# Kernel tuning notes

Measured on AMD Instinct MI355X. Metric: run time of the kernel, lower is better.

The kernel has to match this reference:

```python
import jax, jax.numpy as jnp
import numpy as np

D_MODEL = 1024
N_HEADS = 16


def setup_inputs() -> dict:
    key = jax.random.key(0)
    ks = jax.random.split(key, 5)
    B, T, C = 4, 2048, D_MODEL
    x = jax.random.normal(ks[0], (B, T, C), dtype=jnp.float32)
    W_attn = jax.random.normal(ks[1], (C, 3 * C), dtype=jnp.float32) * (1.0 / np.sqrt(C))
    b_attn = jnp.zeros((3 * C,), dtype=jnp.float32)
    W_proj = jax.random.normal(ks[2], (C, C), dtype=jnp.float32) * (1.0 / np.sqrt(C))
    b_proj = jnp.zeros((C,), dtype=jnp.float32)
    return {"x": x, "W_attn": W_attn, "b_attn": b_attn, "W_proj": W_proj, "b_proj": b_proj}


def reference(x, W_attn, b_attn, W_proj, b_proj):
    B, T, C = x.shape
    H = N_HEADS
    hd = C // H
    qkv = x @ W_attn + b_attn                      # [B,T,3C]
    q, k, v = jnp.split(qkv, 3, axis=2)
    # [B,T,C] -> [B,H,T,hd]
    q = q.reshape(B, T, H, hd).transpose(0, 2, 1, 3)
    k = k.reshape(B, T, H, hd).transpose(0, 2, 1, 3)
    v = v.reshape(B, T, H, hd).transpose(0, 2, 1, 3)
    scale = 1.0 / jnp.sqrt(jnp.float32(hd))
    attn = jnp.einsum('bhqd,bhkd->bhqk', q, k) * scale
    causal = jnp.tril(jnp.ones((T, T), dtype=bool))
    attn = jnp.where(causal[None, None], attn, -jnp.inf)
    w = jax.nn.softmax(attn, axis=-1)
    ctx = jnp.einsum('bhqk,bhkd->bhqd', w, v)      # [B,H,T,hd]
    ctx = ctx.transpose(0, 2, 1, 3).reshape(B, T, C)
    return ctx @ W_proj + b_proj
```

## Files before the change

kernel.cpp:

```cpp
#include <hip/hip_runtime.h>
#include <hip/hip_bf16.h>

typedef __bf16 bf16x8 __attribute__((ext_vector_type(8)));
typedef __bf16 bf16x4 __attribute__((ext_vector_type(4)));
typedef float f32x4 __attribute__((ext_vector_type(4)));

#define MFMA(A, B, C) __builtin_amdgcn_mfma_f32_16x16x32_bf16((A), (B), (C), 0, 0, 0)

#if __has_builtin(__builtin_amdgcn_exp2f)
#define EXP2(x) __builtin_amdgcn_exp2f(x)
#else
#define EXP2(x) exp2f(x)
#endif

#define T_SEQ 2048
#define BATCH 4
#define CDIM  1024
#define HEADS 16
#define HD    64
#define MROWS (BATCH * T_SEQ)
#define QK_SCALE 0.18033688011112042f
#define KTILES (CDIM / 64)

__device__ __forceinline__ void async_ld16(const __bf16* g, __bf16* l) {
    __builtin_amdgcn_global_load_lds(
        (const __attribute__((address_space(1))) void*)g,
        (__attribute__((address_space(3))) void*)l, 16, 0, 0);
}

__global__ __launch_bounds__(256) void prep(const float* __restrict__ x,
                                            __bf16* __restrict__ xbf,
                                            const float* __restrict__ Wa,
                                            __bf16* __restrict__ Wat,
                                            const float* __restrict__ Wp,
                                            __bf16* __restrict__ qkv)
{
    __shared__ float tile[32][33];
    const int bid = blockIdx.x;
    if (bid < 4096) {
        long i = ((long)bid * 256 + threadIdx.x) * 8;
        f32x4 f0 = ((const f32x4*)(x + i))[0];
        f32x4 f1 = ((const f32x4*)(x + i))[1];
        bf16x8 v;
#pragma unroll
        for (int j = 0; j < 4; j++) { v[j] = (__bf16)f0[j]; v[4 + j] = (__bf16)f1[j]; }
        *(bf16x8*)(xbf + i) = v;
    } else if (bid < 7168) {
        const int bb = bid - 4096;
        const int tx = threadIdx.x & 31, ty = threadIdx.x >> 5;
        const int c0 = (bb % 96) * 32, r0 = (bb / 96) * 32;
#pragma unroll
        for (int i = 0; i < 4; i++)
            tile[ty + i * 8][tx] = Wa[(long)(r0 + ty + i * 8) * (3 * CDIM) + c0 + tx];
        __syncthreads();
#pragma unroll
        for (int i = 0; i < 4; i++)
            Wat[(long)(c0 + ty + i * 8) * CDIM + r0 + tx] = (__bf16)tile[tx][ty + i * 8];
    } else {
        const int bb = bid - 7168;
        const int tx = threadIdx.x & 31, ty = threadIdx.x >> 5;
        const int c0 = (bb % 32) * 32, r0 = (bb / 32) * 32;
#pragma unroll
        for (int i = 0; i < 4; i++)
            tile[ty + i * 8][tx] = Wp[(long)(r0 + ty + i * 8) * CDIM + c0 + tx];
        __syncthreads();
#pragma unroll
        for (int i = 0; i < 4; i++)
            qkv[(long)(c0 + ty + i * 8) * (3 * CDIM) + 2 * CDIM + r0 + tx] =
                (__bf16)tile[tx][ty + i * 8];
    }
}


#define QS_ALO(p, kt)                                                            \
    do {                                                                         \
        async_ld16(Asrc + (long)(kt) * 64, &Ab[p][sdst]);                        \
        async_ld16(Asrc + (long)128 * CDIM + (kt) * 64, &Ab[p][8192 + sdst]);    \
    } while (0)
#define QS_AHI(p, kt)                                                            \
    do {                                                                         \
        async_ld16(Asrc + (long)64 * CDIM + (kt) * 64, &Ab[p][4096 + sdst]);     \
        async_ld16(Asrc + (long)192 * CDIM + (kt) * 64, &Ab[p][12288 + sdst]);   \
    } while (0)
#define QS_B(p, kt)                                                              \
    do {                                                                         \
        async_ld16(Bsrc + (long)(kt) * 64, &Bb[p][sdst]);                        \
        async_ld16(Bsrc + (long)64 * CDIM + (kt) * 64, &Bb[p][4096 + sdst]);     \
        async_ld16(Bsrc + (long)128 * CDIM + (kt) * 64, &Bb[p][8192 + sdst]);    \
    } while (0)

__global__ __launch_bounds__(512, 2) void gemm_qkv(const __bf16* __restrict__ A,
                                                   const __bf16* __restrict__ Bt,
                                                   const float* __restrict__ bias,
                                                   __bf16* __restrict__ C,
                                                   __bf16* __restrict__ vt)
{
    __shared__ __attribute__((aligned(16))) __bf16 Ab[2][256 * 64];
    __shared__ __attribute__((aligned(16))) __bf16 Bb[2][192 * 64];

    const int bid = (int)blockIdx.x;
    const int swz = (bid & 7) * 64 + (bid >> 3);
    const int n0 = (swz & 15) * 192;
    const int m0 = (swz >> 4) * 256;

    const int t = threadIdx.x;
    const int wave = t >> 6, lane = t & 63;
    const int quad = lane >> 4, l15 = lane & 15;
    const int wm = wave >> 2, wn = wave & 3;

    const int srow = t >> 3;
    const int scol = ((t & 7) * 8) ^ ((srow & 7) << 3);
    const int sdst = srow * 64 + (t & 7) * 8;
    const __bf16* Asrc = A + (long)(m0 + srow) * CDIM + scol;
    const __bf16* Bsrc = Bt + (long)(n0 + srow) * CDIM + scol;

    const int kx0 = (quad * 8) ^ ((l15 & 7) << 3);
    const int kx1 = (32 + quad * 8) ^ ((l15 & 7) << 3);
    const int aro = (wm * 128 + l15) * 64;
    const int bro = (wn * 48 + l15) * 64;

    f32x4 acc[8][3] = {};
    bf16x8 A0[4][2], A1[4][2], B0[2][2], B1[2];

    QS_ALO(0, 0); QS_AHI(0, 0); QS_B(0, 0);
    QS_ALO(1, 1); QS_AHI(1, 1); QS_B(1, 1);
    asm volatile("s_waitcnt vmcnt(7)" ::: "memory");
    __builtin_amdgcn_s_barrier();
#pragma unroll
    for (int mf = 0; mf < 4; mf++) {
        A0[mf][0] = *(const bf16x8*)&Ab[0][aro + mf * 1024 + kx0];
        A0[mf][1] = *(const bf16x8*)&Ab[0][aro + mf * 1024 + kx1];
    }
#pragma unroll
    for (int nf = 0; nf < 2; nf++) {
        B0[nf][0] = *(const bf16x8*)&Bb[0][bro + nf * 1024 + kx0];
        B0[nf][1] = *(const bf16x8*)&Bb[0][bro + nf * 1024 + kx1];
    }

#pragma unroll 2
    for (int kt = 0; kt < KTILES; ++kt) {
        const int cur = kt & 1, nxt = cur ^ 1;

#pragma unroll
        for (int mf = 0; mf < 4; mf++) {
            A1[mf][0] = *(const bf16x8*)&Ab[cur][aro + 4096 + mf * 1024 + kx0];
            A1[mf][1] = *(const bf16x8*)&Ab[cur][aro + 4096 + mf * 1024 + kx1];
        }
        B1[0] = *(const bf16x8*)&Bb[cur][bro + 2048 + kx0];
        B1[1] = *(const bf16x8*)&Bb[cur][bro + 2048 + kx1];
        asm volatile("s_waitcnt lgkmcnt(10)" ::: "memory");
        __builtin_amdgcn_sched_barrier(0);
        __builtin_amdgcn_s_setprio(1);
#pragma unroll
        for (int mf = 0; mf < 4; mf++)
#pragma unroll
            for (int nf = 0; nf < 2; nf++) {
                acc[mf][nf] = MFMA(A0[mf][0], B0[nf][0], acc[mf][nf]);
                acc[mf][nf] = MFMA(A0[mf][1], B0[nf][1], acc[mf][nf]);
            }
        __builtin_amdgcn_s_setprio(0);
        asm volatile("s_waitcnt lgkmcnt(0)" ::: "memory");
        __builtin_amdgcn_sched_barrier(0);
        __builtin_amdgcn_s_setprio(1);
#pragma unroll
        for (int mf = 0; mf < 4; mf++)
#pragma unroll
            for (int nf = 0; nf < 2; nf++) {
                acc[4 + mf][nf] = MFMA(A1[mf][0], B0[nf][0], acc[4 + mf][nf]);
                acc[4 + mf][nf] = MFMA(A1[mf][1], B0[nf][1], acc[4 + mf][nf]);
            }
        __builtin_amdgcn_s_setprio(0);
        asm volatile("s_waitcnt vmcnt(0)" ::: "memory");
        __builtin_amdgcn_s_barrier();

        __builtin_amdgcn_s_setprio(1);
#pragma unroll
        for (int mf = 0; mf < 4; mf++) {
            acc[mf][2] = MFMA(A0[mf][0], B1[0], acc[mf][2]);
            acc[mf][2] = MFMA(A0[mf][1], B1[1], acc[mf][2]);
        }
        __builtin_amdgcn_s_setprio(0);
        if (kt + 1 < KTILES) {
#pragma unroll
            for (int mf = 0; mf < 4; mf++) {
                A0[mf][0] = *(const bf16x8*)&Ab[nxt][aro + mf * 1024 + kx0];
                A0[mf][1] = *(const bf16x8*)&Ab[nxt][aro + mf * 1024 + kx1];
            }
#pragma unroll
            for (int nf = 0; nf < 2; nf++) {
                B0[nf][0] = *(const bf16x8*)&Bb[nxt][bro + nf * 1024 + kx0];
                B0[nf][1] = *(const bf16x8*)&Bb[nxt][bro + nf * 1024 + kx1];
            }
        }
        if (kt + 2 < KTILES) { QS_ALO(cur, kt + 2); QS_AHI(cur, kt + 2); QS_B(cur, kt + 2); }
        __builtin_amdgcn_s_setprio(1);
#pragma unroll
        for (int mf = 0; mf < 4; mf++) {
            acc[4 + mf][2] = MFMA(A1[mf][0], B1[0], acc[4 + mf][2]);
            acc[4 + mf][2] = MFMA(A1[mf][1], B1[1], acc[4 + mf][2]);
        }
        __builtin_amdgcn_s_setprio(0);
    }

    const int bB = m0 >> 11;
    const int tb = (m0 & (T_SEQ - 1)) + wm * 128;
#pragma unroll
    for (int mf = 0; mf < 8; mf++) {
#pragma unroll
        for (int nf = 0; nf < 3; nf++) {
            const int colb = n0 + wn * 48 + nf * 16;
            const int col = colb + l15;
            const float bv = bias[col];
            if (colb >= 2 * CDIM) {
                __bf16* vdst = vt + (long)(bB * CDIM + col - 2 * CDIM) * T_SEQ
                             + tb + (mf >> 2) * 64 + (mf & 3) * 16 + quad * 4;
                bf16x4 pv;
#pragma unroll
                for (int r = 0; r < 4; r++) pv[r] = (__bf16)(acc[mf][nf][r] + bv);
                *(bf16x4*)vdst = pv;
            } else {
                const float sc = (col < CDIM) ? QK_SCALE : 1.0f;
#pragma unroll
                for (int r = 0; r < 4; r++) {
                    const int row = m0 + wm * 128 + (mf >> 2) * 64 + (mf & 3) * 16 + quad * 4 + r;
                    C[(long)row * (3 * CDIM) + col] = (__bf16)((acc[mf][nf][r] + bv) * sc);
                }
            }
        }
    }
}

#define PS_A(p, kt)                                                              \
    do {                                                                         \
        async_ld16(Asrc + (long)(kt) * 64, &Ab[p][sdst]);                        \
        async_ld16(Asrc + (long)64 * (3 * CDIM) + (kt) * 64, &Ab[p][4096 + sdst]); \
    } while (0)
#define PS_B(p, kt)                                                              \
    do {                                                                         \
        async_ld16(Bsrc + (long)(kt) * 64, &Bb[p][sdst]);                        \
        async_ld16(Bsrc + (long)64 * (3 * CDIM) + (kt) * 64, &Bb[p][4096 + sdst]); \
        async_ld16(Bsrc + (long)128 * (3 * CDIM) + (kt) * 64, &Bb[p][8192 + sdst]); \
        async_ld16(Bsrc + (long)192 * (3 * CDIM) + (kt) * 64, &Bb[p][12288 + sdst]); \
    } while (0)

__global__ __launch_bounds__(512, 2) void gemm_proj(const __bf16* __restrict__ A,
                                                    const float* __restrict__ bias,
                                                    float* __restrict__ C)
{
    __shared__ __attribute__((aligned(16))) __bf16 Ab[2][128 * 64];
    __shared__ __attribute__((aligned(16))) __bf16 Bb[2][256 * 64];

    const int bid = (int)blockIdx.x;
    const int swz = (bid & 7) * 32 + (bid >> 3);
    const int n0 = (swz & 3) * 256;
    const int m0 = (swz >> 2) * 128;

    const int t = threadIdx.x;
    const int wave = t >> 6, lane = t & 63;
    const int quad = lane >> 4, l15 = lane & 15;
    const int wm = wave >> 2, wn = wave & 3;

    const int srow = t >> 3;
    const int scol = ((t & 7) * 8) ^ ((srow & 7) << 3);
    const int sdst = srow * 64 + (t & 7) * 8;
    const __bf16* Asrc = A + (long)(m0 + srow) * (3 * CDIM) + scol;
    const __bf16* Bsrc = A + (long)(n0 + srow) * (3 * CDIM) + 2 * CDIM + scol;

    const int kx0 = (quad * 8) ^ ((l15 & 7) << 3);
    const int kx1 = (32 + quad * 8) ^ ((l15 & 7) << 3);
    const int aro = (wm * 64 + l15) * 64;
    const int bro = (wn * 64 + l15) * 64;

    f32x4 acc[4][4] = {};
    bf16x8 A0[2][2], A1[2][2], B0[2][2], B1[2][2];

    PS_A(0, 0); PS_B(0, 0);
    PS_A(1, 1); PS_B(1, 1);
    asm volatile("s_waitcnt vmcnt(6)" ::: "memory");
    __builtin_amdgcn_s_barrier();
#pragma unroll
    for (int mf = 0; mf < 2; mf++) {
        A0[mf][0] = *(const bf16x8*)&Ab[0][aro + mf * 1024 + kx0];
        A0[mf][1] = *(const bf16x8*)&Ab[0][aro + mf * 1024 + kx1];
    }
#pragma unroll
    for (int nf = 0; nf < 2; nf++) {
        B0[nf][0] = *(const bf16x8*)&Bb[0][bro + nf * 1024 + kx0];
        B0[nf][1] = *(const bf16x8*)&Bb[0][bro + nf * 1024 + kx1];
    }

#pragma unroll 2
    for (int kt = 0; kt < KTILES; ++kt) {
        const int cur = kt & 1, nxt = cur ^ 1;

#pragma unroll
        for (int mf = 0; mf < 2; mf++) {
            A1[mf][0] = *(const bf16x8*)&Ab[cur][aro + 2048 + mf * 1024 + kx0];
            A1[mf][1] = *(const bf16x8*)&Ab[cur][aro + 2048 + mf * 1024 + kx1];
        }
#pragma unroll
        for (int nf = 0; nf < 2; nf++) {
            B1[nf][0] = *(const bf16x8*)&Bb[cur][bro + 2048 + nf * 1024 + kx0];
            B1[nf][1] = *(const bf16x8*)&Bb[cur][bro + 2048 + nf * 1024 + kx1];
        }
        asm volatile("s_waitcnt lgkmcnt(8)" ::: "memory");
        __builtin_amdgcn_sched_barrier(0);
        __builtin_amdgcn_s_setprio(1);
#pragma unroll
        for (int mf = 0; mf < 2; mf++)
#pragma unroll
            for (int nf = 0; nf < 2; nf++) {
                acc[mf][nf] = MFMA(A0[mf][0], B0[nf][0], acc[mf][nf]);
                acc[mf][nf] = MFMA(A0[mf][1], B0[nf][1], acc[mf][nf]);
            }
        __builtin_amdgcn_s_setprio(0);
        asm volatile("s_waitcnt lgkmcnt(0)" ::: "memory");
        __builtin_amdgcn_sched_barrier(0);
        __builtin_amdgcn_s_setprio(1);
#pragma unroll
        for (int mf = 0; mf < 2; mf++)
#pragma unroll
            for (int nf = 0; nf < 2; nf++) {
                acc[2 + mf][nf] = MFMA(A1[mf][0], B0[nf][0], acc[2 + mf][nf]);
                acc[2 + mf][nf] = MFMA(A1[mf][1], B0[nf][1], acc[2 + mf][nf]);
            }
        __builtin_amdgcn_s_setprio(0);
        asm volatile("s_waitcnt vmcnt(0)" ::: "memory");
        __builtin_amdgcn_s_barrier();

        __builtin_amdgcn_s_setprio(1);
#pragma unroll
        for (int mf = 0; mf < 2; mf++)
#pragma unroll
            for (int nf = 0; nf < 2; nf++) {
                acc[mf][2 + nf] = MFMA(A0[mf][0], B1[nf][0], acc[mf][2 + nf]);
                acc[mf][2 + nf] = MFMA(A0[mf][1], B1[nf][1], acc[mf][2 + nf]);
            }
        __builtin_amdgcn_s_setprio(0);
        if (kt + 1 < KTILES) {
#pragma unroll
            for (int mf = 0; mf < 2; mf++) {
                A0[mf][0] = *(const bf16x8*)&Ab[nxt][aro + mf * 1024 + kx0];
                A0[mf][1] = *(const bf16x8*)&Ab[nxt][aro + mf * 1024 + kx1];
            }
#pragma unroll
            for (int nf = 0; nf < 2; nf++) {
                B0[nf][0] = *(const bf16x8*)&Bb[nxt][bro + nf * 1024 + kx0];
                B0[nf][1] = *(const bf16x8*)&Bb[nxt][bro + nf * 1024 + kx1];
            }
        }
        if (kt + 2 < KTILES) { PS_A(cur, kt + 2); PS_B(cur, kt + 2); }
        __builtin_amdgcn_s_setprio(1);
#pragma unroll
        for (int mf = 0; mf < 2; mf++)
#pragma unroll
            for (int nf = 0; nf < 2; nf++) {
                acc[2 + mf][2 + nf] = MFMA(A1[mf][0], B1[nf][0], acc[2 + mf][2 + nf]);
                acc[2 + mf][2 + nf] = MFMA(A1[mf][1], B1[nf][1], acc[2 + mf][2 + nf]);
            }
        __builtin_amdgcn_s_setprio(0);
    }

#pragma unroll
    for (int mf = 0; mf < 4; mf++) {
#pragma unroll
        for (int nf = 0; nf < 4; nf++) {
            const int col = n0 + wn * 64 + (nf >> 1) * 32 + (nf & 1) * 16 + l15;
            const float bv = bias[col];
#pragma unroll
            for (int r = 0; r < 4; r++) {
                const int row = m0 + wm * 64 + (mf >> 1) * 32 + (mf & 1) * 16 + quad * 4 + r;
                C[(long)row * CDIM + col] = acc[mf][nf][r] + bv;
            }
        }
    }
}

__global__ __launch_bounds__(256) void attn_kernel(__bf16* qkv,
                                                   const __bf16* __restrict__ vt)
{
    __shared__ __attribute__((aligned(16))) __bf16 Ks[2][64 * 32];
    __shared__ __attribute__((aligned(16))) __bf16 Vts[2][64 * 32];
    __shared__ __attribute__((aligned(16))) __bf16 Ps[8][16 * 72];

    const int bh = blockIdx.x;
    const int b = bh >> 4, h = bh & 15;
    const int qt = (int)gridDim.y - 1 - (int)blockIdx.y;
    const int q0 = qt * 128;
    const int t = threadIdx.x;
    const int wave = t >> 6, lane = t & 63;
    const int quad = lane >> 4, l15 = lane & 15;

    bf16x8 qfr[2][2];
#pragma unroll
    for (int f = 0; f < 2; f++) {
        const __bf16* qb = qkv + (long)(b * T_SEQ + q0 + f * 64 + wave * 16 + l15) * (3 * CDIM) + h * HD;
        qfr[f][0] = *(const bf16x8*)(qb + quad * 8);
        qfr[f][1] = *(const bf16x8*)(qb + 32 + quad * 8);
    }

    bf16x8 vone;
#pragma unroll
    for (int j = 0; j < 8; j++) vone[j] = (__bf16)1.0f;

    f32x4 Oacc[2][4] = {};
    f32x4 lacc[2] = {};

    const __bf16* kbase = qkv + (long)(b * T_SEQ + (t >> 2)) * (3 * CDIM)
                          + CDIM + h * HD + (t & 3) * 8;
    const __bf16* vbase = vt + ((long)bh * HD + (t >> 2)) * T_SEQ + (t & 3) * 8;

    const int ntiles = (q0 + 128) / 64;
    for (int kt = 0; kt < ntiles; kt++) {
        const __bf16* kp = kbase + (long)kt * 64 * (3 * CDIM);
        async_ld16(kp,      &Ks[0][t * 8]);
        async_ld16(kp + 32, &Ks[1][t * 8]);
        const __bf16* vp = vbase + kt * 64;
        async_ld16(vp,      &Vts[0][t * 8]);
        async_ld16(vp + 32, &Vts[1][t * 8]);
        __syncthreads();

#pragma unroll
        for (int c = 0; c < 4; c++) {
            bf16x8 kf0 = *(const bf16x8*)&Ks[0][(c * 16 + l15) * 32 + quad * 8];
            bf16x8 kf1 = *(const bf16x8*)&Ks[1][(c * 16 + l15) * 32 + quad * 8];
#pragma unroll
            for (int f = 0; f < 2; f++) {
                f32x4 z = {};
                z = MFMA(kf0, qfr[f][0], z);
                z = MFMA(kf1, qfr[f][1], z);
                const int qbf = q0 + f * 64 + wave * 16;
                const int qg = qbf + l15;
                const int kvb = kt * 64 + c * 16 + quad * 4;
                bf16x4 pk;
                if (kt * 64 + 63 > qbf) {
#pragma unroll
                    for (int r = 0; r < 4; r++) {
                        float v = (kvb + r > qg) ? -1e30f : z[r];
                        pk[r] = (__bf16)EXP2(v);
                    }
                } else {
#pragma unroll
                    for (int r = 0; r < 4; r++)
                        pk[r] = (__bf16)EXP2(z[r]);
                }
                *(bf16x4*)&Ps[wave * 2 + f][l15 * 72 + c * 16 + quad * 4] = pk;
            }
        }

        __threadfence_block();

        bf16x8 pf[2][2];
#pragma unroll
        for (int f = 0; f < 2; f++) {
            pf[f][0] = *(const bf16x8*)&Ps[wave * 2 + f][l15 * 72 + quad * 8];
            pf[f][1] = *(const bf16x8*)&Ps[wave * 2 + f][l15 * 72 + 32 + quad * 8];
            lacc[f] = MFMA(pf[f][0], vone, lacc[f]);
            lacc[f] = MFMA(pf[f][1], vone, lacc[f]);
        }
#pragma unroll
        for (int n = 0; n < 4; n++) {
            bf16x8 vf0 = *(const bf16x8*)&Vts[0][(n * 16 + l15) * 32 + quad * 8];
            bf16x8 vf1 = *(const bf16x8*)&Vts[1][(n * 16 + l15) * 32 + quad * 8];
#pragma unroll
            for (int f = 0; f < 2; f++) {
                Oacc[f][n] = MFMA(pf[f][0], vf0, Oacc[f][n]);
                Oacc[f][n] = MFMA(pf[f][1], vf1, Oacc[f][n]);
            }
        }
        __syncthreads();
    }

#pragma unroll
    for (int f = 0; f < 2; f++)
#pragma unroll
        for (int n = 0; n < 4; n++) {
            int col = h * HD + n * 16 + l15;
#pragma unroll
            for (int r = 0; r < 4; r++) {
                int row = q0 + f * 64 + wave * 16 + quad * 4 + r;
                float val = Oacc[f][n][r] / lacc[f][r];
                qkv[(long)(b * T_SEQ + row) * (3 * CDIM) + col] = (__bf16)val;
            }
        }
}

extern "C" void kernel_launch(void* const* d_in, const int* in_sizes, int n_in,
                              void* d_out, int out_size, void* d_ws, size_t ws_size,
                              hipStream_t stream) {
    (void)in_sizes; (void)n_in; (void)out_size; (void)ws_size;
    const float* x  = (const float*)d_in[0];
    const float* Wa = (const float*)d_in[1];
    const float* ba = (const float*)d_in[2];
    const float* Wp = (const float*)d_in[3];
    const float* bp = (const float*)d_in[4];
    float* out = (float*)d_out;

    char* ws = (char*)d_ws;
    __bf16* qkv = (__bf16*)(ws);
    __bf16* vt  = (__bf16*)(ws + 50331648);
    __bf16* xbf = (__bf16*)d_out;
    __bf16* Wat = (__bf16*)((char*)d_out + 16777216);

    prep<<<dim3(8192), 256, 0, stream>>>(x, xbf, Wa, Wat, Wp, qkv);

    gemm_qkv<<<dim3(512), 512, 0, stream>>>(xbf, Wat, ba, qkv, vt);

    attn_kernel<<<dim3(BATCH * HEADS, T_SEQ / 128), 256, 0, stream>>>(qkv, vt);

    gemm_proj<<<dim3(256), 512, 0, stream>>>(qkv, bp, out);
}
```

Measured before the change: 230.6 us.

## Double-buffer K/V tiles in attention kernel with async prefetch two ahead

```diff
diff --git a/kernel.cpp b/kernel.cpp
--- a/kernel.cpp
+++ b/kernel.cpp
@@ -376,11 +376,21 @@
     }
 }
 
-__global__ __launch_bounds__(256) void attn_kernel(__bf16* qkv,
-                                                   const __bf16* __restrict__ vt)
+#define ATT_STAGE(p, kt_)                                                        \
+    do {                                                                         \
+        const __bf16* kp_ = kbase + (long)(kt_) * 64 * (3 * CDIM);               \
+        async_ld16(kp_,      &Ks[p][0][t * 8]);                                  \
+        async_ld16(kp_ + 32, &Ks[p][1][t * 8]);                                  \
+        const __bf16* vp_ = vbase + (kt_) * 64;                                  \
+        async_ld16(vp_,      &Vts[p][0][t * 8]);                                 \
+        async_ld16(vp_ + 32, &Vts[p][1][t * 8]);                                 \
+    } while (0)
+
+__global__ __launch_bounds__(256, 3) void attn_kernel(__bf16* qkv,
+                                                      const __bf16* __restrict__ vt)
 {
-    __shared__ __attribute__((aligned(16))) __bf16 Ks[2][64 * 32];
-    __shared__ __attribute__((aligned(16))) __bf16 Vts[2][64 * 32];
+    __shared__ __attribute__((aligned(16))) __bf16 Ks[2][2][64 * 32];
+    __shared__ __attribute__((aligned(16))) __bf16 Vts[2][2][64 * 32];
     __shared__ __attribute__((aligned(16))) __bf16 Ps[8][16 * 72];
 
     const int bh = blockIdx.x;
@@ -411,19 +421,19 @@
     const __bf16* vbase = vt + ((long)bh * HD + (t >> 2)) * T_SEQ + (t & 3) * 8;
 
     const int ntiles = (q0 + 128) / 64;
+
+    ATT_STAGE(0, 0);
+    ATT_STAGE(1, 1);
+    asm volatile("s_waitcnt vmcnt(4)" ::: "memory");
+    __builtin_amdgcn_s_barrier();
+
     for (int kt = 0; kt < ntiles; kt++) {
-        const __bf16* kp = kbase + (long)kt * 64 * (3 * CDIM);
-        async_ld16(kp,      &Ks[0][t * 8]);
-        async_ld16(kp + 32, &Ks[1][t * 8]);
-        const __bf16* vp = vbase + kt * 64;
-        async_ld16(vp,      &Vts[0][t * 8]);
-        async_ld16(vp + 32, &Vts[1][t * 8]);
-        __syncthreads();
+        const int cur = kt & 1;
 
 #pragma unroll
         for (int c = 0; c < 4; c++) {
-            bf16x8 kf0 = *(const bf16x8*)&Ks[0][(c * 16 + l15) * 32 + quad * 8];
-            bf16x8 kf1 = *(const bf16x8*)&Ks[1][(c * 16 + l15) * 32 + quad * 8];
+            bf16x8 kf0 = *(const bf16x8*)&Ks[cur][0][(c * 16 + l15) * 32 + quad * 8];
+            bf16x8 kf1 = *(const bf16x8*)&Ks[cur][1][(c * 16 + l15) * 32 + quad * 8];
 #pragma unroll
             for (int f = 0; f < 2; f++) {
                 f32x4 z = {};
@@ -455,20 +465,33 @@
         for (int f = 0; f < 2; f++) {
             pf[f][0] = *(const bf16x8*)&Ps[wave * 2 + f][l15 * 72 + quad * 8];
             pf[f][1] = *(const bf16x8*)&Ps[wave * 2 + f][l15 * 72 + 32 + quad * 8];
+        }
+        bf16x8 vf[4][2];
+#pragma unroll
+        for (int n = 0; n < 4; n++) {
+            vf[n][0] = *(const bf16x8*)&Vts[cur][0][(n * 16 + l15) * 32 + quad * 8];
+            vf[n][1] = *(const bf16x8*)&Vts[cur][1][(n * 16 + l15) * 32 + quad * 8];
+        }
+        asm volatile("s_waitcnt lgkmcnt(0)" ::: "memory");
+        __builtin_amdgcn_sched_barrier(0);
+        asm volatile("s_waitcnt vmcnt(0)" ::: "memory");
+        __builtin_amdgcn_s_barrier();
+
+        if (kt + 2 < ntiles) ATT_STAGE(cur, kt + 2);
+        __builtin_amdgcn_s_setprio(1);
+#pragma unroll
+        for (int f = 0; f < 2; f++) {
             lacc[f] = MFMA(pf[f][0], vone, lacc[f]);
             lacc[f] = MFMA(pf[f][1], vone, lacc[f]);
         }
 #pragma unroll
-        for (int n = 0; n < 4; n++) {
-            bf16x8 vf0 = *(const bf16x8*)&Vts[0][(n * 16 + l15) * 32 + quad * 8];
-            bf16x8 vf1 = *(const bf16x8*)&Vts[1][(n * 16 + l15) * 32 + quad * 8];
+        for (int n = 0; n < 4; n++)
 #pragma unroll
             for (int f = 0; f < 2; f++) {
-                Oacc[f][n] = MFMA(pf[f][0], vf0, Oacc[f][n]);
-                Oacc[f][n] = MFMA(pf[f][1], vf1, Oacc[f][n]);
-            }
-        }
-        __syncthreads();
+                Oacc[f][n] = MFMA(pf[f][0], vf[n][0], Oacc[f][n]);
+                Oacc[f][n] = MFMA(pf[f][1], vf[n][1], Oacc[f][n]);
+            }
+        __builtin_amdgcn_s_setprio(0);
     }
 
 #pragma unroll
```

Measured after the change: 229.4 us. No clear change (-0.5%).
